# Kernel optimization log

Hardware: AMD Instinct MI355X
Metric: run time of the kernel (lower is better)

Reference implementation:

```python
import jax, jax.numpy as jnp
import numpy as np

N_NODES = 100000
N_EDGES = 1600000
IN_CH, HID_CH, OUT_CH = 128, 64, 64


def setup_inputs() -> dict:
    key = jax.random.key(0)
    k1, k2, k3, k4 = jax.random.split(key, 4)
    x = jax.random.normal(k1, (N_NODES, IN_CH), dtype=jnp.float32)
    edge_index = jax.random.randint(k2, (2, N_EDGES), 0, N_NODES, dtype=jnp.int64)
    # Glorot-style init for GCNConv linear weights; zero bias (PyG default)
    W1 = jax.random.normal(k3, (IN_CH, HID_CH), dtype=jnp.float32) * (1.0 / np.sqrt(IN_CH))
    b1 = jnp.zeros((HID_CH,), dtype=jnp.float32)
    W2 = jax.random.normal(k4, (HID_CH, OUT_CH), dtype=jnp.float32) * (1.0 / np.sqrt(HID_CH))
    b2 = jnp.zeros((OUT_CH,), dtype=jnp.float32)
    return {"x": x, "edge_index": edge_index, "W1": W1, "b1": b1, "W2": W2, "b2": b2}


def gcn_conv(x, row, col, W, b):
    # PyG GCNConv: linear transform, then sym-normalized scatter-add aggregation
    h = x @ W  # [N, out]
    ones = jnp.ones(col.shape, dtype=h.dtype)
    deg = jax.ops.segment_sum(ones, col, num_segments=N_NODES)  # in-degree incl. self-loops
    dinv = jnp.where(deg > 0, jax.lax.rsqrt(deg), 0.0)
    norm = dinv[row] * dinv[col]  # [E+N]
    msg = h[row] * norm[:, None]  # gather + scale, [E+N, out]
    out = jax.ops.segment_sum(msg, col, num_segments=N_NODES)  # scatter-add
    return out + b


def reference(x, edge_index, W1, b1, W2, b2):
    # add self-loops once (same edge set for both layers)
    loops = jnp.arange(N_NODES, dtype=edge_index.dtype)
    row = jnp.concatenate([edge_index[0], loops])
    col = jnp.concatenate([edge_index[1], loops])
    h = jax.nn.relu(gcn_conv(x, row, col, W1, b1))
    return gcn_conv(h, row, col, W2, b2)
```

## Files before the change

### kernel.cpp

```cpp
#include <hip/hip_runtime.h>


#define BKT_SH 7
#define BKT_CAP 4096
#define CHUNK 6144
#define BM 128
#define BK 32

__device__ __forceinline__ unsigned short f2bf(float f) {
    unsigned u = __builtin_bit_cast(unsigned, f);
    u = (u + 0x7FFF + ((u >> 16) & 1)) >> 16;
    return (unsigned short)u;
}
__device__ __forceinline__ float bflo(unsigned u) {
    return __builtin_bit_cast(float, u << 16);
}
__device__ __forceinline__ float bfhi(unsigned u) {
    return __builtin_bit_cast(float, u & 0xFFFF0000u);
}

__global__ __launch_bounds__(256) void k_zero_i(int* __restrict__ p, int n) {
    int i = blockIdx.x * 256 + threadIdx.x;
    if (i < n) p[i] = 0;
}

__global__ __launch_bounds__(256) void k_bin(const int* __restrict__ row,
                                             const int* __restrict__ col,
                                             int* __restrict__ cursor,
                                             unsigned* __restrict__ bentries,
                                             int E) {
    __shared__ unsigned sorted[CHUNK];
    __shared__ unsigned short bof[CHUNK];
    __shared__ int hist[1024];
    __shared__ int ex0[1024];
    __shared__ int cur[1024];
    __shared__ int gbase[1024];
    __shared__ int tsum[256];
    int b = blockIdx.x, t = threadIdx.x;
    int s0 = b * CHUNK;
    int cnt = E - s0; if (cnt > CHUNK) cnt = CHUNK;

    for (int i = t; i < 1024; i += 256) hist[i] = 0;
    __syncthreads();
    for (int i = t; i < cnt; i += 256)
        atomicAdd(&hist[col[s0 + i] >> BKT_SH], 1);
    __syncthreads();
    {
        int b0 = hist[4 * t], b1 = hist[4 * t + 1], b2 = hist[4 * t + 2], b3 = hist[4 * t + 3];
        int tot = b0 + b1 + b2 + b3;
        tsum[t] = tot;
        __syncthreads();
#pragma unroll
        for (int d = 1; d < 256; d <<= 1) {
            int x = (t >= d) ? tsum[t - d] : 0;
            __syncthreads();
            tsum[t] += (t >= d) ? x : 0;
            __syncthreads();
        }
        int ex = tsum[t] - tot;
        ex0[4 * t] = ex;
        ex0[4 * t + 1] = ex + b0;
        ex0[4 * t + 2] = ex + b0 + b1;
        ex0[4 * t + 3] = ex + b0 + b1 + b2;
        cur[4 * t] = ex0[4 * t];
        cur[4 * t + 1] = ex0[4 * t + 1];
        cur[4 * t + 2] = ex0[4 * t + 2];
        cur[4 * t + 3] = ex0[4 * t + 3];
    }
    __syncthreads();
    for (int i = t; i < 1024; i += 256)
        if (hist[i] > 0) gbase[i] = i * BKT_CAP + atomicAdd(&cursor[i], hist[i]);
    for (int i = t; i < cnt; i += 256) {
        int c = col[s0 + i], r = row[s0 + i];
        int bkt = c >> BKT_SH;
        int p = atomicAdd(&cur[bkt], 1);
        sorted[p] = ((unsigned)(c & ((1 << BKT_SH) - 1)) << 17) | (unsigned)r;
        bof[p] = (unsigned short)bkt;
    }
    __syncthreads();
    for (int i = t; i < cnt; i += 256) {
        int bkt = bof[i];
        int pos = gbase[bkt] + (i - ex0[bkt]);
        if (pos < (bkt + 1) * BKT_CAP) bentries[pos] = sorted[i];
    }
}

__global__ __launch_bounds__(256) void k_bucket_sort(
    unsigned* __restrict__ bentries, const int* __restrict__ cursor,
    int* __restrict__ start, int* __restrict__ cntarr,
    float* __restrict__ dinv, int N) {
    __shared__ int hist[128];
    __shared__ int incl[128];
    __shared__ int cur[128];
    __shared__ int rows[BKT_CAP];
    int b = blockIdx.x, t = threadIdx.x;
    int base = b * BKT_CAP;
    int cnt = cursor[b];
    if (cnt > BKT_CAP) cnt = BKT_CAP;

    if (t < 128) hist[t] = 0;
    __syncthreads();
    for (int i = t; i < cnt; i += 256)
        atomicAdd(&hist[bentries[base + i] >> 17], 1);
    __syncthreads();
    if (t < 128) incl[t] = hist[t];
    __syncthreads();
#pragma unroll
    for (int d = 1; d < 128; d <<= 1) {
        int x = (t < 128 && t >= d) ? incl[t - d] : 0;
        __syncthreads();
        if (t < 128 && t >= d) incl[t] += x;
        __syncthreads();
    }
    if (t < 128) {
        int ex = incl[t] - hist[t];
        int node = (b << BKT_SH) + t;
        if (node < N) {
            start[node] = base + ex;
            cntarr[node] = hist[t];
            dinv[node] = rsqrtf((float)hist[t] + 1.0f);
        }
        cur[t] = ex;
    }
    __syncthreads();
    for (int i = t; i < cnt; i += 256) {
        unsigned en = bentries[base + i];
        int p = atomicAdd(&cur[en >> 17], 1);
        rows[p] = (int)(en & 0x1FFFF);
    }
    __syncthreads();
    for (int i = t; i < cnt; i += 256) bentries[base + i] = (unsigned)rows[i];
}

__global__ __launch_bounds__(256) void k_gemm_f32in(
    const float* __restrict__ X, const float* __restrict__ W,
    const float* __restrict__ dinv, unsigned short* __restrict__ outb,
    int N, int K) {
    __shared__ float Xs[BK][BM + 4];
    __shared__ float Ws[BK][64];
    int t = threadIdx.x;
    int bm = blockIdx.x * BM;
    int tm = t >> 4, tn = t & 15;

    float acc[8][4];
#pragma unroll
    for (int i = 0; i < 8; ++i)
#pragma unroll
        for (int j = 0; j < 4; ++j) acc[i][j] = 0.f;

    for (int kb = 0; kb < K; kb += BK) {
#pragma unroll
        for (int it = 0; it < 4; ++it) {
            int r = (t >> 3) + 32 * it;
            int grow = bm + r;
            int k4 = t & 7;
            float4 v = make_float4(0.f, 0.f, 0.f, 0.f);
            if (grow < N) v = *(const float4*)(X + (size_t)grow * K + kb + k4 * 4);
            Xs[k4 * 4 + 0][r] = v.x;
            Xs[k4 * 4 + 1][r] = v.y;
            Xs[k4 * 4 + 2][r] = v.z;
            Xs[k4 * 4 + 3][r] = v.w;
        }
#pragma unroll
        for (int it = 0; it < 2; ++it) {
            int idx = t + 256 * it;
            ((float4*)Ws)[idx] = ((const float4*)(W + (size_t)kb * 64))[idx];
        }
        __syncthreads();
#pragma unroll
        for (int k = 0; k < BK; ++k) {
            float4 xa = *(const float4*)&Xs[k][tm * 8];
            float4 xb = *(const float4*)&Xs[k][tm * 8 + 4];
            float4 w = *(const float4*)&Ws[k][tn * 4];
            float xs[8] = {xa.x, xa.y, xa.z, xa.w, xb.x, xb.y, xb.z, xb.w};
#pragma unroll
            for (int i = 0; i < 8; ++i) {
                acc[i][0] = fmaf(xs[i], w.x, acc[i][0]);
                acc[i][1] = fmaf(xs[i], w.y, acc[i][1]);
                acc[i][2] = fmaf(xs[i], w.z, acc[i][2]);
                acc[i][3] = fmaf(xs[i], w.w, acc[i][3]);
            }
        }
        __syncthreads();
    }
#pragma unroll
    for (int i = 0; i < 8; ++i) {
        int grow = bm + tm * 8 + i;
        if (grow < N) {
            float s = dinv[grow];
            ushort4 v;
            v.x = f2bf(acc[i][0] * s);
            v.y = f2bf(acc[i][1] * s);
            v.z = f2bf(acc[i][2] * s);
            v.w = f2bf(acc[i][3] * s);
            *(ushort4*)(outb + (size_t)grow * 64 + tn * 4) = v;
        }
    }
}

__global__ __launch_bounds__(256) void k_gemm_bf16in(
    const unsigned short* __restrict__ Xb, const float* __restrict__ W,
    const float* __restrict__ dinv, unsigned short* __restrict__ outb,
    int N, int K) {
    __shared__ float Xs[BK][BM + 4];
    __shared__ float Ws[BK][64];
    int t = threadIdx.x;
    int bm = blockIdx.x * BM;
    int tm = t >> 4, tn = t & 15;

    float acc[8][4];
#pragma unroll
    for (int i = 0; i < 8; ++i)
#pragma unroll
        for (int j = 0; j < 4; ++j) acc[i][j] = 0.f;

    for (int kb = 0; kb < K; kb += BK) {
#pragma unroll
        for (int it = 0; it < 2; ++it) {
            int idx = t * 2 + it;
            int r = idx >> 2;
            int q = idx & 3;
            int grow = bm + r;
            uint4 v = make_uint4(0u, 0u, 0u, 0u);
            if (grow < N) v = *(const uint4*)(Xb + (size_t)grow * K + kb + q * 8);
            int k0 = q * 8;
            Xs[k0 + 0][r] = bflo(v.x); Xs[k0 + 1][r] = bfhi(v.x);
            Xs[k0 + 2][r] = bflo(v.y); Xs[k0 + 3][r] = bfhi(v.y);
            Xs[k0 + 4][r] = bflo(v.z); Xs[k0 + 5][r] = bfhi(v.z);
            Xs[k0 + 6][r] = bflo(v.w); Xs[k0 + 7][r] = bfhi(v.w);
        }
#pragma unroll
        for (int it = 0; it < 2; ++it) {
            int idx = t + 256 * it;
            ((float4*)Ws)[idx] = ((const float4*)(W + (size_t)kb * 64))[idx];
        }
        __syncthreads();
#pragma unroll
        for (int k = 0; k < BK; ++k) {
            float4 xa = *(const float4*)&Xs[k][tm * 8];
            float4 xb = *(const float4*)&Xs[k][tm * 8 + 4];
            float4 w = *(const float4*)&Ws[k][tn * 4];
            float xs[8] = {xa.x, xa.y, xa.z, xa.w, xb.x, xb.y, xb.z, xb.w};
#pragma unroll
            for (int i = 0; i < 8; ++i) {
                acc[i][0] = fmaf(xs[i], w.x, acc[i][0]);
                acc[i][1] = fmaf(xs[i], w.y, acc[i][1]);
                acc[i][2] = fmaf(xs[i], w.z, acc[i][2]);
                acc[i][3] = fmaf(xs[i], w.w, acc[i][3]);
            }
        }
        __syncthreads();
    }
#pragma unroll
    for (int i = 0; i < 8; ++i) {
        int grow = bm + tm * 8 + i;
        if (grow < N) {
            float s = dinv[grow];
            ushort4 v;
            v.x = f2bf(acc[i][0] * s);
            v.y = f2bf(acc[i][1] * s);
            v.z = f2bf(acc[i][2] * s);
            v.w = f2bf(acc[i][3] * s);
            *(ushort4*)(outb + (size_t)grow * 64 + tn * 4) = v;
        }
    }
}

__global__ __launch_bounds__(256) void k_gather(
    const uint4* __restrict__ srcq, const int* __restrict__ eros,
    const int* __restrict__ start, const int* __restrict__ cntarr,
    const float* __restrict__ dinv, const float* __restrict__ bias,
    float* __restrict__ dstf, uint4* __restrict__ dstq, int N, int mode) {
    int idx = blockIdx.x * 256 + threadIdx.x;
    int node = idx >> 3;
    if (node >= N) return;
    int l = idx & 7;

    uint4 sv = srcq[(size_t)node * 8 + l];
    float a0 = bflo(sv.x), a1 = bfhi(sv.x);
    float a2 = bflo(sv.y), a3 = bfhi(sv.y);
    float a4 = bflo(sv.z), a5 = bfhi(sv.z);
    float a6 = bflo(sv.w), a7 = bfhi(sv.w);

    int e = start[node];
    int eend = e + cntarr[node];
    for (; e + 8 <= eend; e += 8) {
        uint4 v[8];
#pragma unroll
        for (int j = 0; j < 8; ++j) {
            int r = eros[e + j];
            v[j] = srcq[(size_t)r * 8 + l];
        }
#pragma unroll
        for (int j = 0; j < 8; ++j) {
            a0 += bflo(v[j].x); a1 += bfhi(v[j].x);
            a2 += bflo(v[j].y); a3 += bfhi(v[j].y);
            a4 += bflo(v[j].z); a5 += bfhi(v[j].z);
            a6 += bflo(v[j].w); a7 += bfhi(v[j].w);
        }
    }
    for (; e + 4 <= eend; e += 4) {
        uint4 v[4];
#pragma unroll
        for (int j = 0; j < 4; ++j) {
            int r = eros[e + j];
            v[j] = srcq[(size_t)r * 8 + l];
        }
#pragma unroll
        for (int j = 0; j < 4; ++j) {
            a0 += bflo(v[j].x); a1 += bfhi(v[j].x);
            a2 += bflo(v[j].y); a3 += bfhi(v[j].y);
            a4 += bflo(v[j].z); a5 += bfhi(v[j].z);
            a6 += bflo(v[j].w); a7 += bfhi(v[j].w);
        }
    }
    for (; e < eend; ++e) {
        int r = eros[e];
        uint4 v = srcq[(size_t)r * 8 + l];
        a0 += bflo(v.x); a1 += bfhi(v.x);
        a2 += bflo(v.y); a3 += bfhi(v.y);
        a4 += bflo(v.z); a5 += bfhi(v.z);
        a6 += bflo(v.w); a7 += bfhi(v.w);
    }
    float sc = dinv[node];
    const float4* bp = (const float4*)bias;
    float4 b0 = bp[l * 2], b1 = bp[l * 2 + 1];
    a0 = a0 * sc + b0.x; a1 = a1 * sc + b0.y;
    a2 = a2 * sc + b0.z; a3 = a3 * sc + b0.w;
    a4 = a4 * sc + b1.x; a5 = a5 * sc + b1.y;
    a6 = a6 * sc + b1.z; a7 = a7 * sc + b1.w;
    if (mode) {
        a0 = fmaxf(a0, 0.f); a1 = fmaxf(a1, 0.f);
        a2 = fmaxf(a2, 0.f); a3 = fmaxf(a3, 0.f);
        a4 = fmaxf(a4, 0.f); a5 = fmaxf(a5, 0.f);
        a6 = fmaxf(a6, 0.f); a7 = fmaxf(a7, 0.f);
        uint4 o;
        o.x = (unsigned)f2bf(a0) | ((unsigned)f2bf(a1) << 16);
        o.y = (unsigned)f2bf(a2) | ((unsigned)f2bf(a3) << 16);
        o.z = (unsigned)f2bf(a4) | ((unsigned)f2bf(a5) << 16);
        o.w = (unsigned)f2bf(a6) | ((unsigned)f2bf(a7) << 16);
        dstq[(size_t)node * 8 + l] = o;
    } else {
        float4 o0 = make_float4(a0, a1, a2, a3);
        float4 o1 = make_float4(a4, a5, a6, a7);
        float4* d = (float4*)(dstf + (size_t)node * 64 + l * 8);
        d[0] = o0;
        d[1] = o1;
    }
}

extern "C" void kernel_launch(void* const* d_in, const int* in_sizes, int n_in,
                              void* d_out, int out_size, void* d_ws, size_t ws_size,
                              hipStream_t stream) {
    const float* x = (const float*)d_in[0];
    const int* ei = (const int*)d_in[1];
    const float* W1 = (const float*)d_in[2];
    const float* b1 = (const float*)d_in[3];
    const float* W2 = (const float*)d_in[4];
    const float* b2 = (const float*)d_in[5];

    int N = in_sizes[0] / 128;
    int E = in_sizes[1] / 2;
    const int* row = ei;
    const int* col = ei + E;
    int nb = (N + (1 << BKT_SH) - 1) >> BKT_SH;

    char* ws = (char*)d_ws;
    int* cursor = (int*)ws;
    int* start = (int*)(ws + (1 << 16));
    int* cntarr = (int*)(ws + (1 << 19));
    float* dinv = (float*)(ws + 960 * 1024);
    unsigned* bentries = (unsigned*)(ws + (2 << 20));
    unsigned short* Ab = (unsigned short*)(ws + (15 << 20));
    unsigned short* Hb = (unsigned short*)d_out;
    float* OUTF = (float*)d_out;

    int gemmblk = (N + BM - 1) / BM;
    int binblk = (E + CHUNK - 1) / CHUNK;
    int gblk = (N * 8 + 255) / 256;

    k_zero_i<<<(nb + 255) / 256, 256, 0, stream>>>(cursor, nb);
    k_bin<<<binblk, 256, 0, stream>>>(row, col, cursor, bentries, E);
    k_bucket_sort<<<nb, 256, 0, stream>>>(bentries, cursor, start, cntarr, dinv, N);

    k_gemm_f32in<<<gemmblk, 256, 0, stream>>>(x, W1, dinv, Ab, N, 128);
    k_gather<<<gblk, 256, 0, stream>>>((const uint4*)Ab, (const int*)bentries,
                                       start, cntarr, dinv, b1,
                                       nullptr, (uint4*)Hb, N, 1);

    k_gemm_bf16in<<<gemmblk, 256, 0, stream>>>(Hb, W2, dinv, Ab, N, 64);
    k_gather<<<gblk, 256, 0, stream>>>((const uint4*)Ab, (const int*)bentries,
                                       start, cntarr, dinv, b2,
                                       OUTF, nullptr, N, 0);
}
```

Measured before the change: 244.6 us.

## Split bf16 node features into 16-wide slices and gather per slice

```diff
diff --git a/kernel.cpp b/kernel.cpp
--- a/kernel.cpp
+++ b/kernel.cpp
@@ -6,6 +6,9 @@
 #define CHUNK 6144
 #define BM 128
 #define BK 32
+
+typedef unsigned nuint4 __attribute__((ext_vector_type(4)));
+typedef float nfloat4 __attribute__((ext_vector_type(4)));
 
 __device__ __forceinline__ unsigned short f2bf(float f) {
     unsigned u = __builtin_bit_cast(unsigned, f);
@@ -87,8 +90,7 @@
 
 __global__ __launch_bounds__(256) void k_bucket_sort(
     unsigned* __restrict__ bentries, const int* __restrict__ cursor,
-    int* __restrict__ start, int* __restrict__ cntarr,
-    float* __restrict__ dinv, int N) {
+    unsigned* __restrict__ scnt, float* __restrict__ dinv, int N) {
     __shared__ int hist[128];
     __shared__ int incl[128];
     __shared__ int cur[128];
@@ -116,8 +118,8 @@
         int ex = incl[t] - hist[t];
         int node = (b << BKT_SH) + t;
         if (node < N) {
-            start[node] = base + ex;
-            cntarr[node] = hist[t];
+            int h = hist[t] > 127 ? 127 : hist[t];
+            scnt[node] = ((unsigned)(base + ex) << 7) | (unsigned)h;
             dinv[node] = rsqrtf((float)hist[t] + 1.0f);
         }
         cur[t] = ex;
@@ -183,17 +185,18 @@
         }
         __syncthreads();
     }
+    int s = tn >> 2;
 #pragma unroll
     for (int i = 0; i < 8; ++i) {
         int grow = bm + tm * 8 + i;
         if (grow < N) {
-            float s = dinv[grow];
+            float sc = dinv[grow];
             ushort4 v;
-            v.x = f2bf(acc[i][0] * s);
-            v.y = f2bf(acc[i][1] * s);
-            v.z = f2bf(acc[i][2] * s);
-            v.w = f2bf(acc[i][3] * s);
-            *(ushort4*)(outb + (size_t)grow * 64 + tn * 4) = v;
+            v.x = f2bf(acc[i][0] * sc);
+            v.y = f2bf(acc[i][1] * sc);
+            v.z = f2bf(acc[i][2] * sc);
+            v.w = f2bf(acc[i][3] * sc);
+            *(ushort4*)(outb + ((size_t)s * N + grow) * 16 + (tn & 3) * 4) = v;
         }
     }
 }
@@ -214,15 +217,17 @@
 #pragma unroll
         for (int j = 0; j < 4; ++j) acc[i][j] = 0.f;
 
+    const uint4* Xq = (const uint4*)Xb;
     for (int kb = 0; kb < K; kb += BK) {
 #pragma unroll
         for (int it = 0; it < 2; ++it) {
             int idx = t * 2 + it;
             int r = idx >> 2;
             int q = idx & 3;
+            int qq = (kb >> 3) + q;
             int grow = bm + r;
             uint4 v = make_uint4(0u, 0u, 0u, 0u);
-            if (grow < N) v = *(const uint4*)(Xb + (size_t)grow * K + kb + q * 8);
+            if (grow < N) v = Xq[((size_t)(qq >> 1) * N + grow) * 2 + (qq & 1)];
             int k0 = q * 8;
             Xs[k0 + 0][r] = bflo(v.x); Xs[k0 + 1][r] = bfhi(v.x);
             Xs[k0 + 2][r] = bflo(v.y); Xs[k0 + 3][r] = bfhi(v.y);
@@ -251,45 +256,54 @@
         }
         __syncthreads();
     }
+    int s = tn >> 2;
 #pragma unroll
     for (int i = 0; i < 8; ++i) {
         int grow = bm + tm * 8 + i;
         if (grow < N) {
-            float s = dinv[grow];
+            float sc = dinv[grow];
             ushort4 v;
-            v.x = f2bf(acc[i][0] * s);
-            v.y = f2bf(acc[i][1] * s);
-            v.z = f2bf(acc[i][2] * s);
-            v.w = f2bf(acc[i][3] * s);
-            *(ushort4*)(outb + (size_t)grow * 64 + tn * 4) = v;
+            v.x = f2bf(acc[i][0] * sc);
+            v.y = f2bf(acc[i][1] * sc);
+            v.z = f2bf(acc[i][2] * sc);
+            v.w = f2bf(acc[i][3] * sc);
+            *(ushort4*)(outb + ((size_t)s * N + grow) * 16 + (tn & 3) * 4) = v;
         }
     }
 }
 
 __global__ __launch_bounds__(256) void k_gather(
     const uint4* __restrict__ srcq, const int* __restrict__ eros,
-    const int* __restrict__ start, const int* __restrict__ cntarr,
-    const float* __restrict__ dinv, const float* __restrict__ bias,
-    float* __restrict__ dstf, uint4* __restrict__ dstq, int N, int mode) {
-    int idx = blockIdx.x * 256 + threadIdx.x;
-    int node = idx >> 3;
+    const unsigned* __restrict__ scnt, const float* __restrict__ bias,
+    float* __restrict__ dstf, uint4* __restrict__ dstq,
+    int N, int nchunks, int mode) {
+    int b = blockIdx.x, t = threadIdx.x;
+    int s = (b & 7) >> 1;
+    int chunk = (b >> 3) * 2 + (b & 1);
+    if (chunk >= nchunks) return;
+    int node = chunk * 128 + (t >> 1);
     if (node >= N) return;
-    int l = idx & 7;
-
-    uint4 sv = srcq[(size_t)node * 8 + l];
+    int l = t & 1;
+
+    const uint4* su4 = srcq + (size_t)s * N * 2;
+
+    uint4 sv = su4[(size_t)node * 2 + l];
     float a0 = bflo(sv.x), a1 = bfhi(sv.x);
     float a2 = bflo(sv.y), a3 = bfhi(sv.y);
     float a4 = bflo(sv.z), a5 = bfhi(sv.z);
     float a6 = bflo(sv.w), a7 = bfhi(sv.w);
 
-    int e = start[node];
-    int eend = e + cntarr[node];
+    unsigned sc_pack = scnt[node];
+    int e = (int)(sc_pack >> 7);
+    int cnt = (int)(sc_pack & 127u);
+    float sc = rsqrtf((float)cnt + 1.0f);
+    int eend = e + cnt;
     for (; e + 8 <= eend; e += 8) {
         uint4 v[8];
 #pragma unroll
         for (int j = 0; j < 8; ++j) {
-            int r = eros[e + j];
-            v[j] = srcq[(size_t)r * 8 + l];
+            int r = __builtin_nontemporal_load(&eros[e + j]);
+            v[j] = su4[(size_t)r * 2 + l];
         }
 #pragma unroll
         for (int j = 0; j < 8; ++j) {
@@ -303,8 +317,8 @@
         uint4 v[4];
 #pragma unroll
         for (int j = 0; j < 4; ++j) {
-            int r = eros[e + j];
-            v[j] = srcq[(size_t)r * 8 + l];
+            int r = __builtin_nontemporal_load(&eros[e + j]);
+            v[j] = su4[(size_t)r * 2 + l];
         }
 #pragma unroll
         for (int j = 0; j < 4; ++j) {
@@ -315,16 +329,15 @@
         }
     }
     for (; e < eend; ++e) {
-        int r = eros[e];
-        uint4 v = srcq[(size_t)r * 8 + l];
+        int r = __builtin_nontemporal_load(&eros[e]);
+        uint4 v = su4[(size_t)r * 2 + l];
         a0 += bflo(v.x); a1 += bfhi(v.x);
         a2 += bflo(v.y); a3 += bfhi(v.y);
         a4 += bflo(v.z); a5 += bfhi(v.z);
         a6 += bflo(v.w); a7 += bfhi(v.w);
     }
-    float sc = dinv[node];
     const float4* bp = (const float4*)bias;
-    float4 b0 = bp[l * 2], b1 = bp[l * 2 + 1];
+    float4 b0 = bp[s * 4 + l * 2], b1 = bp[s * 4 + l * 2 + 1];
     a0 = a0 * sc + b0.x; a1 = a1 * sc + b0.y;
     a2 = a2 * sc + b0.z; a3 = a3 * sc + b0.w;
     a4 = a4 * sc + b1.x; a5 = a5 * sc + b1.y;
@@ -334,18 +347,19 @@
         a2 = fmaxf(a2, 0.f); a3 = fmaxf(a3, 0.f);
         a4 = fmaxf(a4, 0.f); a5 = fmaxf(a5, 0.f);
         a6 = fmaxf(a6, 0.f); a7 = fmaxf(a7, 0.f);
-        uint4 o;
+        nuint4 o;
         o.x = (unsigned)f2bf(a0) | ((unsigned)f2bf(a1) << 16);
         o.y = (unsigned)f2bf(a2) | ((unsigned)f2bf(a3) << 16);
         o.z = (unsigned)f2bf(a4) | ((unsigned)f2bf(a5) << 16);
         o.w = (unsigned)f2bf(a6) | ((unsigned)f2bf(a7) << 16);
-        dstq[(size_t)node * 8 + l] = o;
+        nuint4* dp = (nuint4*)&dstq[((size_t)s * N + node) * 2 + l];
+        __builtin_nontemporal_store(o, dp);
     } else {
-        float4 o0 = make_float4(a0, a1, a2, a3);
-        float4 o1 = make_float4(a4, a5, a6, a7);
-        float4* d = (float4*)(dstf + (size_t)node * 64 + l * 8);
-        d[0] = o0;
-        d[1] = o1;
+        nfloat4* d = (nfloat4*)(dstf + (size_t)node * 64 + s * 16 + l * 8);
+        nfloat4 o0 = {a0, a1, a2, a3};
+        nfloat4 o1 = {a4, a5, a6, a7};
+        __builtin_nontemporal_store(o0, d);
+        __builtin_nontemporal_store(o1, d + 1);
     }
 }
 
@@ -364,12 +378,12 @@
     const int* row = ei;
     const int* col = ei + E;
     int nb = (N + (1 << BKT_SH) - 1) >> BKT_SH;
+    int nchunks = (N + 127) / 128;
 
     char* ws = (char*)d_ws;
     int* cursor = (int*)ws;
-    int* start = (int*)(ws + (1 << 16));
-    int* cntarr = (int*)(ws + (1 << 19));
-    float* dinv = (float*)(ws + 960 * 1024);
+    unsigned* scnt = (unsigned*)(ws + (1 << 16));
+    float* dinv = (float*)(ws + (1 << 19));
     unsigned* bentries = (unsigned*)(ws + (2 << 20));
     unsigned short* Ab = (unsigned short*)(ws + (15 << 20));
     unsigned short* Hb = (unsigned short*)d_out;
@@ -377,19 +391,17 @@
 
     int gemmblk = (N + BM - 1) / BM;
     int binblk = (E + CHUNK - 1) / CHUNK;
-    int gblk = (N * 8 + 255) / 256;
+    int gblk = ((nchunks + 1) / 2) * 8;
 
     k_zero_i<<<(nb + 255) / 256, 256, 0, stream>>>(cursor, nb);
     k_bin<<<binblk, 256, 0, stream>>>(row, col, cursor, bentries, E);
-    k_bucket_sort<<<nb, 256, 0, stream>>>(bentries, cursor, start, cntarr, dinv, N);
+    k_bucket_sort<<<nb, 256, 0, stream>>>(bentries, cursor, scnt, dinv, N);
 
     k_gemm_f32in<<<gemmblk, 256, 0, stream>>>(x, W1, dinv, Ab, N, 128);
     k_gather<<<gblk, 256, 0, stream>>>((const uint4*)Ab, (const int*)bentries,
-                                       start, cntarr, dinv, b1,
-                                       nullptr, (uint4*)Hb, N, 1);
+                                       scnt, b1, nullptr, (uint4*)Hb, N, nchunks, 1);
 
     k_gemm_bf16in<<<gemmblk, 256, 0, stream>>>(Hb, W2, dinv, Ab, N, 64);
     k_gather<<<gblk, 256, 0, stream>>>((const uint4*)Ab, (const int*)bentries,
-                                       start, cntarr, dinv, b2,
-                                       OUTF, nullptr, N, 0);
-}
+                                       scnt, b2, OUTF, nullptr, N, nchunks, 0);
+}
```

Result: slower. 302.3 us (+23.6%).
